# Performance work log

Hardware: AMD Instinct MI355X
Metric: run time of the kernel (lower is better)

## Reference

```python
import jax, jax.numpy as jnp
import numpy as np


def hilbert_perm(M: int) -> np.ndarray:
    """Permutation ordering the first M cells of a Hilbert curve on a 2^k x 2^k grid."""
    side = 1
    while side * side < M:
        side *= 2
    idx = np.arange(M)
    x = (idx % side).astype(np.int64)
    y = (idx // side).astype(np.int64)
    d = np.zeros(M, dtype=np.int64)
    s = side // 2
    while s > 0:
        rx = ((x & s) > 0).astype(np.int64)
        ry = ((y & s) > 0).astype(np.int64)
        d += s * s * ((3 * rx) ^ ry)
        swap = ry == 0
        flip = swap & (rx == 1)
        x2 = np.where(flip, s - 1 - x, x)
        y2 = np.where(flip, s - 1 - y, y)
        x, y = np.where(swap, y2, x2), np.where(swap, x2, y2)
        s //= 2
    return np.argsort(d, kind='stable')


SEGMENT_SIZE = 512


def setup_inputs() -> dict:
    key = jax.random.key(0)
    ks = jax.random.split(key, 5)
    B, M, H, D = 2, 8192, 8, 64
    hd = H * D  # 512
    q = jax.random.normal(ks[0], (B, M, H, D), dtype=jnp.float32)
    k = jax.random.normal(ks[1], (B, M, H, D), dtype=jnp.float32)
    v = jax.random.normal(ks[2], (B, M, H, D), dtype=jnp.float32)
    w_qkv = jax.random.normal(ks[3], (3 * hd, hd), dtype=jnp.float32) * (hd ** -0.5)
    w_out = jax.random.normal(ks[4], (hd, hd), dtype=jnp.float32) * (hd ** -0.5)
    return {"q": q, "k": k, "v": v, "w_qkv": w_qkv, "w_out": w_out}


def reference(q, k, v, w_qkv, w_out):
    B, M, H, D = q.shape
    hd = H * D
    S = SEGMENT_SIZE
    n_seg = M // S
    # Wrapper: mean over heads, then channel-repeat to hidden_dim
    x = q.mean(axis=2)                       # [B, M, D]
    x = jnp.tile(x, (1, 1, H))               # [B, M, hd]
    # HilbertAttentionCore: fused QKV projection
    qkv = jnp.einsum('bmc,fc->bmf', x, w_qkv)  # [B, M, 3*hd]
    qh, kh, vh = jnp.split(qkv, 3, axis=-1)
    # Hilbert-curve reordering (static permutation of seq dim)
    perm = jnp.asarray(hilbert_perm(M))
    inv = jnp.argsort(perm)
    def seg(t):
        t = t[:, perm]                       # reorder seq
        return t.reshape(B, n_seg, S, H, D)
    qs, ks_, vs = seg(qh), seg(kh), seg(vh)
    scale = D ** -0.5
    scores = jnp.einsum('bnshd,bnthd->bnhst', qs, ks_) * scale  # [B,n_seg,H,S,S]
    attn = jax.nn.softmax(scores, axis=-1)
    out = jnp.einsum('bnhst,bnthd->bnshd', attn, vs)            # [B,n_seg,S,H,D]
    out = out.reshape(B, M, hd)[:, inv]      # undo Hilbert ordering
    out = jnp.einsum('bmc,fc->bmf', out, w_out)  # output projection
    return out.reshape(B, M, H, D)
```

## Files before the change

### kernel.cpp

```cpp
#include <hip/hip_runtime.h>


typedef short bfrag __attribute__((ext_vector_type(8)));
typedef float ffrag __attribute__((ext_vector_type(4)));
typedef short svec4 __attribute__((ext_vector_type(4)));
typedef unsigned uvec4 __attribute__((ext_vector_type(4)));

__device__ inline short f2bf(float x) {
  unsigned u = __builtin_bit_cast(unsigned, x);
  u = (u + 0x7fffu + ((u >> 16) & 1u)) >> 16;
  return (short)u;
}
__device__ inline float fexp2(float x) {
#if __has_builtin(__builtin_amdgcn_exp2f)
  return __builtin_amdgcn_exp2f(x);
#else
  return __expf(x * 0.6931471805599453f);
#endif
}
__device__ inline unsigned cvtpk(float a, float b) {
  unsigned r;
  asm("v_cvt_pk_bf16_f32 %0, %1, %2" : "=v"(r) : "v"(a), "v"(b));
  return r;
}
__device__ inline void gload_lds16(const void* g, void* l) {
  __builtin_amdgcn_global_load_lds(
      (const __attribute__((address_space(1))) unsigned*)g,
      (__attribute__((address_space(3))) unsigned*)l, 16, 0, 0);
}

__device__ inline int d2xy128(int d) {
  int x = 0, y = 0, t = d;
  for (int s = 1; s < 128; s <<= 1) {
    int rx = 1 & (t >> 1);
    int ry = 1 & (t ^ rx);
    if (ry == 0) {
      if (rx == 1) { x = s - 1 - x; y = s - 1 - y; }
      int tt = x; x = y; y = tt;
    }
    x += s * rx;
    y += s * ry;
    t >>= 2;
  }
  return y * 128 + x;
}

__global__ __launch_bounds__(256) void prep_kernel(
    const float* __restrict__ q, const float* __restrict__ w_qkv,
    const float* __restrict__ w_out, short* __restrict__ xmean,
    short* __restrict__ weff, short* __restrict__ woutb,
    int* __restrict__ perm) {
  int i = blockIdx.x * 256 + threadIdx.x;
  if (i < 1048576) {
    int bm = i >> 6, d = i & 63;
    const float* p = q + (size_t)bm * 512 + d;
    float s = 0.f;
#pragma unroll
    for (int h = 0; h < 8; ++h) s += p[h * 64];
    xmean[i] = f2bf(s * 0.125f);
  } else if (i < 1048576 + 98304) {
    int j = i - 1048576;
    int f = j >> 6;
    const float* p = w_qkv + (size_t)f * 512 + (j & 63);
    float s = 0.f;
#pragma unroll
    for (int r = 0; r < 8; ++r) s += p[r * 64];
    if (f < 512) s *= 0.125f * 1.44269504088896f;
    weff[j] = f2bf(s);
  } else if (i < 1048576 + 98304 + 262144) {
    int j = i - 1048576 - 98304;
    woutb[j] = f2bf(w_out[j]);
  } else if (i < 1048576 + 98304 + 262144 + 8192) {
    int r = i - (1048576 + 98304 + 262144);
    perm[r] = d2xy128(r < 4096 ? r : r + 8192);
  }
}

__global__ __launch_bounds__(256, 2) void qkv_kernel(
    const short* __restrict__ xmean, const short* __restrict__ weff,
    const int* __restrict__ perm, short* __restrict__ Qs,
    short* __restrict__ Ks, short* __restrict__ Vt) {
  __shared__ short Wlds[384 * 64];
  __shared__ short Sb[4][2][16 * 72];
  int tid = threadIdx.x;
  int w = tid >> 6, lane = tid & 63;
  int ml = lane & 15, quad = lane >> 4;
  int rg = blockIdx.x >> 2, fq = blockIdx.x & 3;
  int r0 = rg * 64 + w * 16;
  int r = r0 + ml;
  int b = r >> 13, p = r & 8191;
  int src = (b << 13) + perm[p];
  bfrag a0 = *(const bfrag*)(xmean + (size_t)src * 64 + quad * 8);
  bfrag a1 = *(const bfrag*)(xmean + (size_t)src * 64 + 32 + quad * 8);
  int p0 = r0 & 8191;
  int bq = r0 >> 13;
  int nseg = p0 >> 9;
  int sbase = (p0 & 511) + quad * 4;

  {
    int lrow = lane >> 3;
    int lu = lane & 7;
    const short* wsrc = weff + (size_t)(fq * 384 + w * 96 + lrow) * 64 +
                        ((lu ^ (lrow & 7)) * 8);
#pragma unroll
    for (int i = 0; i < 12; ++i)
      gload_lds16(wsrc + (size_t)i * 8 * 64,
                  (char*)Wlds + w * 12288 + i * 1024);
  }
  __syncthreads();

#pragma unroll 1
  for (int gg = 0; gg < 6; ++gg) {
    int nt0 = fq * 24 + gg * 4;
    int f0g = nt0 * 16;
    short* sb = &Sb[w][gg & 1][0];
    if (f0g < 1024) {
#pragma unroll
      for (int t = 0; t < 4; ++t) {
        int row = (gg * 4 + t) * 16 + ml;
        const char* Wb = (const char*)Wlds + row * 128;
        int sw = (row & 7) << 4;
        bfrag wf0 = *(const bfrag*)(Wb + ((quad << 4) ^ sw));
        bfrag wf1 = *(const bfrag*)(Wb + (((4 + quad) << 4) ^ sw));
        ffrag acc = {0.f, 0.f, 0.f, 0.f};
        acc = __builtin_amdgcn_mfma_f32_16x16x32_bf16(wf0, a0, acc, 0, 0, 0);
        acc = __builtin_amdgcn_mfma_f32_16x16x32_bf16(wf1, a1, acc, 0, 0, 0);
        svec4 pk;
#pragma unroll
        for (int g = 0; g < 4; ++g) pk[g] = f2bf(acc[g]);
        *(svec4*)((char*)sb + ml * 144 + t * 32 + quad * 8) = pk;
      }
      __builtin_amdgcn_sched_barrier(0);
      int rrow = lane >> 3;
      int cu = lane & 7;
      bfrag v0 = *(const bfrag*)((char*)sb + rrow * 144 + cu * 16);
      bfrag v1 = *(const bfrag*)((char*)sb + (rrow + 8) * 144 + cu * 16);
      short* dst = (f0g < 512) ? Qs : Ks;
      int fo = f0g & 511;
      *(bfrag*)(dst + (size_t)(r0 + rrow) * 512 + fo + cu * 8) = v0;
      *(bfrag*)(dst + (size_t)(r0 + rrow + 8) * 512 + fo + cu * 8) = v1;
    } else {
#pragma unroll
      for (int t = 0; t < 4; ++t) {
        int nt = nt0 + t;
        int row = (gg * 4 + t) * 16 + ml;
        const char* Wb = (const char*)Wlds + row * 128;
        int sw = (row & 7) << 4;
        bfrag wf0 = *(const bfrag*)(Wb + ((quad << 4) ^ sw));
        bfrag wf1 = *(const bfrag*)(Wb + (((4 + quad) << 4) ^ sw));
        ffrag acc = {0.f, 0.f, 0.f, 0.f};
        acc = __builtin_amdgcn_mfma_f32_16x16x32_bf16(a0, wf0, acc, 0, 0, 0);
        acc = __builtin_amdgcn_mfma_f32_16x16x32_bf16(a1, wf1, acc, 0, 0, 0);
        int fl = nt * 16 + ml - 1024;
        int hh = fl >> 6, dd = fl & 63;
        svec4 pk;
#pragma unroll
        for (int g = 0; g < 4; ++g) pk[g] = f2bf(acc[g]);
        *(svec4*)(Vt + ((((size_t)bq * 16 + nseg) * 8 + hh) * 64 + dd) * 512 +
                  sbase) = pk;
      }
    }
  }
}

__global__ __launch_bounds__(256, 2) void attn_kernel(
    const short* __restrict__ Qs, const short* __restrict__ Ks,
    const short* __restrict__ Vt, const int* __restrict__ perm,
    short* __restrict__ aout) {
  __shared__ short Klds[2][64 * 64];
  __shared__ short Vlds[2][64 * 64];
  int tid = threadIdx.x;
  int w = tid >> 6, lane = tid & 63;
  int ml = lane & 15, quad = lane >> 4;
  int sh = blockIdx.x & 255;
  int qq = blockIdx.x >> 8;
  int b = sh >> 7;
  int n = (sh >> 3) & 15;
  int h = sh & 7;
  size_t segrow = (size_t)(b * 8192 + n * 512);
  const short* Qseg = Qs + segrow * 512 + h * 64;
  const short* Kseg = Ks + segrow * 512 + h * 64;
  const short* Vseg = Vt + (((size_t)(b * 16 + n) * 8 + h) * 64) * 512;
  int q0 = qq * 256 + w * 64;
  bfrag qa[4][2];
#pragma unroll
  for (int nq = 0; nq < 4; ++nq)
#pragma unroll
    for (int ks = 0; ks < 2; ++ks)
      qa[nq][ks] = *(const bfrag*)(Qseg + (size_t)(q0 + nq * 16 + ml) * 512 +
                                   ks * 32 + quad * 8);
  ffrag o[4][4];
  float lrun[4] = {0.f, 0.f, 0.f, 0.f};
#pragma unroll
  for (int nq = 0; nq < 4; ++nq)
#pragma unroll
    for (int dt = 0; dt < 4; ++dt) o[nq][dt] = (ffrag){0.f, 0.f, 0.f, 0.f};

  int srow = lane >> 3;
  int sug = (lane & 7) ^ srow;

  auto stage = [&](int buf, int t0) {
    char* Kd = (char*)&Klds[buf][0] + w * 2048;
    char* Vd = (char*)&Vlds[buf][0] + w * 2048;
    gload_lds16(Kseg + (size_t)(t0 + w * 16 + srow) * 512 + sug * 8, Kd);
    gload_lds16(Kseg + (size_t)(t0 + w * 16 + 8 + srow) * 512 + sug * 8,
                Kd + 1024);
    gload_lds16(Vseg + (size_t)(w * 16 + srow) * 512 + t0 + sug * 8, Vd);
    gload_lds16(Vseg + (size_t)(w * 16 + 8 + srow) * 512 + t0 + sug * 8,
                Vd + 1024);
  };

  auto body = [&](int buf) {
    const char* Kb = (const char*)&Klds[buf][0];
    const char* Vb = (const char*)&Vlds[buf][0];
#pragma unroll
    for (int s = 0; s < 2; ++s) {
      bfrag kk[2][2], vv[4];
#pragma unroll
      for (int mt = 0; mt < 2; ++mt)
#pragma unroll
        for (int ks = 0; ks < 2; ++ks) {
          int row = s * 32 + mt * 16 + ml;
          int byte = row * 128 + ks * 64 + quad * 16;
          kk[mt][ks] = *(const bfrag*)(Kb + (byte ^ ((row & 7) << 4)));
        }
#pragma unroll
      for (int dt = 0; dt < 4; ++dt) {
        int row = dt * 16 + ml;
        int byte = row * 128 + s * 64 + quad * 16;
        vv[dt] = *(const bfrag*)(Vb + (byte ^ ((row & 7) << 4)));
      }
#pragma unroll
      for (int nq = 0; nq < 4; ++nq) {
        ffrag c0 = {0.f, 0.f, 0.f, 0.f}, c1 = {0.f, 0.f, 0.f, 0.f};
        c0 = __builtin_amdgcn_mfma_f32_16x16x32_bf16(kk[0][0], qa[nq][0], c0, 0, 0, 0);
        c0 = __builtin_amdgcn_mfma_f32_16x16x32_bf16(kk[0][1], qa[nq][1], c0, 0, 0, 0);
        c1 = __builtin_amdgcn_mfma_f32_16x16x32_bf16(kk[1][0], qa[nq][0], c1, 0, 0, 0);
        c1 = __builtin_amdgcn_mfma_f32_16x16x32_bf16(kk[1][1], qa[nq][1], c1, 0, 0, 0);
        float e0 = fexp2(c0[0]), e1 = fexp2(c0[1]);
        float e2 = fexp2(c0[2]), e3 = fexp2(c0[3]);
        float e4 = fexp2(c1[0]), e5 = fexp2(c1[1]);
        float e6 = fexp2(c1[2]), e7 = fexp2(c1[3]);
        lrun[nq] += ((e0 + e1) + (e2 + e3)) + ((e4 + e5) + (e6 + e7));
        unsigned A0 = cvtpk(e0, e1), A1 = cvtpk(e2, e3);
        unsigned A2 = cvtpk(e4, e5), A3 = cvtpk(e6, e7);
        asm("v_permlane32_swap_b32 %0, %1" : "+v"(A0), "+v"(A2));
        asm("v_permlane16_swap_b32 %0, %1" : "+v"(A0), "+v"(A2));
        asm("v_permlane32_swap_b32 %0, %1" : "+v"(A1), "+v"(A3));
        asm("v_permlane16_swap_b32 %0, %1" : "+v"(A1), "+v"(A3));
        uvec4 pu;
        pu[0] = A0;
        pu[1] = A1;
        pu[2] = A2;
        pu[3] = A3;
        bfrag pa = __builtin_bit_cast(bfrag, pu);
#pragma unroll
        for (int dt = 0; dt < 4; ++dt)
          o[nq][dt] = __builtin_amdgcn_mfma_f32_16x16x32_bf16(vv[dt], pa,
                                                              o[nq][dt], 0, 0, 0);
      }
    }
  };

  stage(0, 0);
  stage(1, 64);
#pragma unroll 1
  for (int jj = 0; jj < 7; ++jj) {
    asm volatile("s_waitcnt vmcnt(4)" ::: "memory");
    __builtin_amdgcn_s_barrier();
    body(jj & 1);
    if (jj < 6) {
      __builtin_amdgcn_s_barrier();
      stage(jj & 1, (jj + 2) * 64);
    }
  }
  asm volatile("s_waitcnt vmcnt(0)" ::: "memory");
  __builtin_amdgcn_s_barrier();
  body(1);

#pragma unroll
  for (int nq = 0; nq < 4; ++nq) {
    float l = lrun[nq];
    l += __shfl_xor(l, 16);
    l += __shfl_xor(l, 32);
    float inv = 1.f / l;
    int sout = q0 + nq * 16 + ml;
    int om = perm[n * 512 + sout];
    size_t base = ((size_t)(b * 8192 + om)) * 512 + h * 64;
#pragma unroll
    for (int dt = 0; dt < 4; ++dt) {
      svec4 pk;
#pragma unroll
      for (int g = 0; g < 4; ++g) pk[g] = f2bf(o[nq][dt][g] * inv);
      *(svec4*)(aout + base + dt * 16 + quad * 4) = pk;
    }
  }
}

__global__ __launch_bounds__(256, 2) void proj_kernel(
    const short* __restrict__ aout, const short* __restrict__ woutb,
    float* __restrict__ out) {
  __shared__ short As[2][128 * 64];
  __shared__ short Bs[2][128 * 64];
  int tid = threadIdx.x;
  int w = tid >> 6, lane = tid & 63;
  int ml = lane & 15, quad = lane >> 4;
  int rb = blockIdx.x & 127;
  int cb = blockIdx.x >> 7;
  int r0 = rb * 128, c0 = cb * 128;
  int wr = (w >> 1) * 64, wc = (w & 1) * 64;

  ffrag acc[4][4];
#pragma unroll
  for (int m = 0; m < 4; ++m)
#pragma unroll
    for (int n = 0; n < 4; ++n) acc[m][n] = (ffrag){0.f, 0.f, 0.f, 0.f};

  int srow = w * 32 + (lane >> 3);
  int scol = (lane & 7) * 8;
  const short* gA = aout + (size_t)(r0 + srow) * 512 + scol;
  const short* gB = woutb + (size_t)(c0 + srow) * 512 + scol;

  auto stage = [&](int buf, int k0) {
#pragma unroll
    for (int i = 0; i < 4; ++i) {
      gload_lds16(gA + (size_t)i * 8 * 512 + k0,
                  (char*)&As[buf][0] + w * 4096 + i * 1024);
      gload_lds16(gB + (size_t)i * 8 * 512 + k0,
                  (char*)&Bs[buf][0] + w * 4096 + i * 1024);
    }
  };
  auto compute = [&](int buf) {
#pragma unroll
    for (int kk = 0; kk < 2; ++kk) {
      bfrag af[4], bf[4];
#pragma unroll
      for (int m = 0; m < 4; ++m)
        af[m] = *(const bfrag*)&As[buf][(wr + m * 16 + ml) * 64 + kk * 32 +
                                        quad * 8];
#pragma unroll
      for (int n = 0; n < 4; ++n)
        bf[n] = *(const bfrag*)&Bs[buf][(wc + n * 16 + ml) * 64 + kk * 32 +
                                        quad * 8];
#pragma unroll
      for (int m = 0; m < 4; ++m)
#pragma unroll
        for (int n = 0; n < 4; ++n)
          acc[m][n] = __builtin_amdgcn_mfma_f32_16x16x32_bf16(bf[n], af[m],
                                                              acc[m][n], 0, 0, 0);
    }
  };

  stage(0, 0);
  stage(1, 64);
#pragma unroll 1
  for (int t = 0; t < 7; ++t) {
    asm volatile("s_waitcnt vmcnt(8)" ::: "memory");
    __builtin_amdgcn_s_barrier();
    compute(t & 1);
    if (t < 6) {
      __builtin_amdgcn_s_barrier();
      stage(t & 1, (t + 2) * 64);
    }
  }
  asm volatile("s_waitcnt vmcnt(0)" ::: "memory");
  __builtin_amdgcn_s_barrier();
  compute(1);

#pragma unroll
  for (int m = 0; m < 4; ++m)
#pragma unroll
    for (int n = 0; n < 4; ++n)
      *(ffrag*)(out + (size_t)(r0 + wr + m * 16 + ml) * 512 + c0 + wc +
                n * 16 + quad * 4) = acc[m][n];
}

extern "C" void kernel_launch(void* const* d_in, const int* in_sizes, int n_in,
                              void* d_out, int out_size, void* d_ws,
                              size_t ws_size, hipStream_t stream) {
  const float* q = (const float*)d_in[0];
  const float* w_qkv = (const float*)d_in[3];
  const float* w_out = (const float*)d_in[4];
  float* out = (float*)d_out;

  char* ws = (char*)d_ws;
  int* perm = (int*)ws;
  short* xmean = (short*)(ws + 32768);
  short* weff = (short*)(ws + 2129920);
  short* woutb = (short*)(ws + 2326528);
  short* Qs = (short*)(ws + 2850816);
  short* Ks = (short*)(ws + 19628032);
  short* Vt = (short*)(ws + 36405248);
  short* aout = (short*)(ws + 53182464);

  prep_kernel<<<5536, 256, 0, stream>>>(q, w_qkv, w_out, xmean, weff, woutb,
                                        perm);
  qkv_kernel<<<1024, 256, 0, stream>>>(xmean, weff, perm, Qs, Ks, Vt);
  attn_kernel<<<512, 256, 0, stream>>>(Qs, Ks, Vt, perm, aout);
  proj_kernel<<<512, 256, 0, stream>>>(aout, woutb, out);
}
```

Baseline: 183.3 us.

## Move inverse Hilbert gather into projection loads and coalesce V-transpose stores

The attention kernel now writes its output in Hilbert order, contiguous rows, instead of scattering rows through perm. The projection kernel gathers A rows through a new inverse-permutation table built in the prep kernel. The qkv kernel stages V tiles through shared memory so the transposed Vt stores write 4 contiguous sequence positions per lane along each d row. This trades scattered writes for gathered 16-byte loads, and adds a small inv table plus extra LDS round-trips.

Result: no change. 181.3 us (-1.1%).

```diff
diff --git a/kernel.cpp b/kernel.cpp
--- a/kernel.cpp
+++ b/kernel.cpp
@@ -49,7 +49,7 @@
     const float* __restrict__ q, const float* __restrict__ w_qkv,
     const float* __restrict__ w_out, short* __restrict__ xmean,
     short* __restrict__ weff, short* __restrict__ woutb,
-    int* __restrict__ perm) {
+    int* __restrict__ perm, int* __restrict__ inv) {
   int i = blockIdx.x * 256 + threadIdx.x;
   if (i < 1048576) {
     int bm = i >> 6, d = i & 63;
@@ -72,7 +72,9 @@
     woutb[j] = f2bf(w_out[j]);
   } else if (i < 1048576 + 98304 + 262144 + 8192) {
     int r = i - (1048576 + 98304 + 262144);
-    perm[r] = d2xy128(r < 4096 ? r : r + 8192);
+    int v = d2xy128(r < 4096 ? r : r + 8192);
+    perm[r] = v;
+    inv[v] = r;
   }
 }
 
@@ -95,7 +97,6 @@
   int p0 = r0 & 8191;
   int bq = r0 >> 13;
   int nseg = p0 >> 9;
-  int sbase = (p0 & 511) + quad * 4;
 
   {
     int lrow = lane >> 3;
@@ -142,7 +143,6 @@
     } else {
 #pragma unroll
       for (int t = 0; t < 4; ++t) {
-        int nt = nt0 + t;
         int row = (gg * 4 + t) * 16 + ml;
         const char* Wb = (const char*)Wlds + row * 128;
         int sw = (row & 7) << 4;
@@ -151,14 +151,24 @@
         ffrag acc = {0.f, 0.f, 0.f, 0.f};
         acc = __builtin_amdgcn_mfma_f32_16x16x32_bf16(a0, wf0, acc, 0, 0, 0);
         acc = __builtin_amdgcn_mfma_f32_16x16x32_bf16(a1, wf1, acc, 0, 0, 0);
-        int fl = nt * 16 + ml - 1024;
+        svec4 pk;
+#pragma unroll
+        for (int g = 0; g < 4; ++g) pk[g] = f2bf(acc[g]);
+        *(svec4*)((char*)sb + ((t * 16 + ml) * 16 + quad * 4) * 2) = pk;
+      }
+      __builtin_amdgcn_sched_barrier(0);
+      int pos4 = (lane & 3) * 4;
+      int ddl = lane >> 2;
+#pragma unroll
+      for (int rr = 0; rr < 4; ++rr) {
+        int dd64 = rr * 16 + ddl;
+        svec4 v = *(const svec4*)((char*)sb + (dd64 * 16 + pos4) * 2);
+        int fl = f0g + dd64 - 1024;
         int hh = fl >> 6, dd = fl & 63;
-        svec4 pk;
-#pragma unroll
-        for (int g = 0; g < 4; ++g) pk[g] = f2bf(acc[g]);
         *(svec4*)(Vt + ((((size_t)bq * 16 + nseg) * 8 + hh) * 64 + dd) * 512 +
-                  sbase) = pk;
+                  (p0 & 511) + pos4) = v;
       }
+      __builtin_amdgcn_sched_barrier(0);
     }
   }
 }
@@ -283,15 +293,14 @@
     float l = lrun[nq];
     l += __shfl_xor(l, 16);
     l += __shfl_xor(l, 32);
-    float inv = 1.f / l;
+    float inv_l = 1.f / l;
     int sout = q0 + nq * 16 + ml;
-    int om = perm[n * 512 + sout];
-    size_t base = ((size_t)(b * 8192 + om)) * 512 + h * 64;
+    size_t base = ((size_t)(b * 8192 + n * 512 + sout)) * 512 + h * 64;
 #pragma unroll
     for (int dt = 0; dt < 4; ++dt) {
       svec4 pk;
 #pragma unroll
-      for (int g = 0; g < 4; ++g) pk[g] = f2bf(o[nq][dt][g] * inv);
+      for (int g = 0; g < 4; ++g) pk[g] = f2bf(o[nq][dt][g] * inv_l);
       *(svec4*)(aout + base + dt * 16 + quad * 4) = pk;
     }
   }
@@ -299,7 +308,7 @@
 
 __global__ __launch_bounds__(256, 2) void proj_kernel(
     const short* __restrict__ aout, const short* __restrict__ woutb,
-    float* __restrict__ out) {
+    const int* __restrict__ inv, float* __restrict__ out) {
   __shared__ short As[2][128 * 64];
   __shared__ short Bs[2][128 * 64];
   int tid = threadIdx.x;
@@ -316,16 +325,20 @@
 #pragma unroll
     for (int n = 0; n < 4; ++n) acc[m][n] = (ffrag){0.f, 0.f, 0.f, 0.f};
 
-  int srow = w * 32 + (lane >> 3);
   int scol = (lane & 7) * 8;
-  const short* gA = aout + (size_t)(r0 + srow) * 512 + scol;
-  const short* gB = woutb + (size_t)(c0 + srow) * 512 + scol;
+  const short* gAr[4];
+#pragma unroll
+  for (int i = 0; i < 4; ++i) {
+    int grow = r0 + w * 32 + (lane >> 3) + i * 8;
+    int prow = (grow & ~8191) | inv[grow & 8191];
+    gAr[i] = aout + (size_t)prow * 512 + scol;
+  }
+  const short* gB = woutb + (size_t)(c0 + w * 32 + (lane >> 3)) * 512 + scol;
 
   auto stage = [&](int buf, int k0) {
 #pragma unroll
     for (int i = 0; i < 4; ++i) {
-      gload_lds16(gA + (size_t)i * 8 * 512 + k0,
-                  (char*)&As[buf][0] + w * 4096 + i * 1024);
+      gload_lds16(gAr[i] + k0, (char*)&As[buf][0] + w * 4096 + i * 1024);
       gload_lds16(gB + (size_t)i * 8 * 512 + k0,
                   (char*)&Bs[buf][0] + w * 4096 + i * 1024);
     }
@@ -392,10 +405,11 @@
   short* Ks = (short*)(ws + 19628032);
   short* Vt = (short*)(ws + 36405248);
   short* aout = (short*)(ws + 53182464);
+  int* inv = (int*)(ws + 69959680);
 
   prep_kernel<<<5536, 256, 0, stream>>>(q, w_qkv, w_out, xmean, weff, woutb,
-                                        perm);
+                                        perm, inv);
   qkv_kernel<<<1024, 256, 0, stream>>>(xmean, weff, perm, Qs, Ks, Vt);
   attn_kernel<<<512, 256, 0, stream>>>(Qs, Ks, Vt, perm, aout);
-  proj_kernel<<<512, 256, 0, stream>>>(aout, woutb, out);
-}
+  proj_kernel<<<512, 256, 0, stream>>>(aout, woutb, inv, out);
+}
```
